# Kernel optimization log

Measured on AMD Instinct MI355X. Metric: run time of the kernel, lower is better.

## Reference

```python
import jax, jax.numpy as jnp
import numpy as np

# pywt Wavelet('db4') decomposition filters (8 taps)
DEC_LO = jnp.array([-0.010597401784997278, 0.032883011666982945, 0.030841381835986965,
                    -0.18703481171888114, -0.02798376941698385, 0.6308807679295904,
                    0.7148465705525415, 0.23037781330885523], dtype=jnp.float32)
DEC_HI = jnp.array([-0.23037781330885523, 0.7148465705525415, -0.6308807679295904,
                    -0.02798376941698385, 0.18703481171888114, 0.030841381835986965,
                    -0.032883011666982945, -0.010597401784997278], dtype=jnp.float32)
FLEN = 8
LEVEL = 3


def _dwt_last(x, f):
    """Single-level DWT along last axis, pywt 'symmetric' mode.
    out[i] = sum_k f[k] * ext[2i+1-k] (true convolution, downsample by 2)."""
    p = FLEN - 1
    pad = [(0, 0)] * (x.ndim - 1) + [(p, p)]
    xp = jnp.pad(x, pad, mode='symmetric')[..., 1:]
    n = x.shape[-1]
    out_len = (n + FLEN - 1) // 2
    f_rev = f[::-1]
    y = f_rev[0] * xp[..., 0:2 * out_len:2]
    for j in range(1, FLEN):  # fixed 8-tap loop
        y = y + f_rev[j] * xp[..., j:j + 2 * out_len:2]
    return y


def _dwt_h(x, f):
    # DWT along axis -2 (rows/H)
    return jnp.swapaxes(_dwt_last(jnp.swapaxes(x, -1, -2), f), -1, -2)


def _dwt2(x):
    # x: [B, H, W] -> (cA, cH, cV, cD), matching pywt dwt2 ('aa','da','ad','dd')
    lo_w = _dwt_last(x, DEC_LO)
    hi_w = _dwt_last(x, DEC_HI)
    cA = _dwt_h(lo_w, DEC_LO)  # low H,  low W
    cH = _dwt_h(lo_w, DEC_HI)  # high H, low W  (horizontal detail)
    cV = _dwt_h(hi_w, DEC_LO)  # low H,  high W (vertical detail)
    cD = _dwt_h(hi_w, DEC_HI)  # high H, high W (diagonal detail)
    return cA, cH, cV, cD


def setup_inputs() -> dict:
    key = jax.random.key(0)
    x = jax.random.normal(key, (16, 1, 1024, 1024), dtype=jnp.float32)
    return {"x": x}


def reference(x):
    # wavedec2 ordering: (cA_L, (cH_L, cV_L, cD_L), ..., (cH_1, cV_1, cD_1))
    a = x[:, 0]  # [B, H, W]
    details = []
    for _ in range(LEVEL):
        a, lh, hl, hh = _dwt2(a)
        details.insert(0, (lh, hl, hh))  # coarsest first, as pywt returns
    outs = [a[:, None]]  # [B,1,h,w]
    for lh, hl, hh in details:
        outs += [lh[:, None], hl[:, None], hh[:, None]]
    return tuple(outs)
```

## Files before the change

### kernel.cpp

```cpp
#include <hip/hip_runtime.h>

#define NT 512

__device__ __forceinline__ int refl(int i, int n) {
    i = (i < 0) ? (-i - 1) : i;
    i = (i >= n) ? (2 * n - 1 - i) : i;
    return i;
}

__device__ __forceinline__ unsigned bpack(float lo, float hi) {
    union { float f; unsigned u; } a, b;
    a.f = lo; b.f = hi;
    const unsigned ua = (a.u + 0x7FFFu + ((a.u >> 16) & 1u)) >> 16;
    const unsigned ub = (b.u + 0x7FFFu + ((b.u >> 16) & 1u)) & 0xFFFF0000u;
    return ua | ub;
}
__device__ __forceinline__ float b_lo(unsigned u) {
    union { unsigned u; float f; } x; x.u = u << 16; return x.f;
}
__device__ __forceinline__ float b_hi(unsigned u) {
    union { unsigned u; float f; } x; x.u = u & 0xFFFF0000u; return x.f;
}

__global__ __launch_bounds__(NT, 8)
void dwt2_fused(const float* __restrict__ in, int n, int ldin, int inb,
                int m, int nty, int ntx,
                float* __restrict__ oA, int ldA, int Ab,
                float* __restrict__ oH, float* __restrict__ oV,
                float* __restrict__ oD)
{
    constexpr float LOF[8] = {
        -0.010597401784997278f,  0.032883011666982945f,
         0.030841381835986965f, -0.18703481171888114f,
        -0.02798376941698385f,   0.6308807679295904f,
         0.7148465705525415f,    0.23037781330885523f };
    constexpr float HIF[8] = {
        -0.23037781330885523f,   0.7148465705525415f,
        -0.6308807679295904f,   -0.02798376941698385f,
         0.18703481171888114f,   0.030841381835986965f,
        -0.032883011666982945f, -0.010597401784997278f };

    __shared__ unsigned s[70 * 36];

    const int G = gridDim.x;
    const int q = G >> 3, rm = G & 7;
    const int xcd = blockIdx.x & 7, pos = blockIdx.x >> 3;
    const int i = xcd * q + (xcd < rm ? xcd : rm) + pos;
    const int ty = i % nty;
    const int t2 = i / nty;
    const int tx = t2 % ntx;
    const int b  = t2 / ntx;

    const int tid = threadIdx.x;
    const int c0 = tx * 32, r0 = ty * 32;
    const float* Ain = in + b * inb;

    const int rb  = 2 * r0 - 6;
    const int cw0 = 2 * c0 - 8;

    const bool interior = (rb >= 0) && (rb + 69 < n) && (cw0 >= 0) && (cw0 + 71 < n);

    const int tr0 = tid >> 3, g0 = tid & 7;
    const bool has2 = (tid < 48);
    const int tr1 = 64 + (tid >> 3), g1 = tid & 7;

    float v0[16], v1[16];
    if (interior) {
        const float* p0 = Ain + (rb + tr0) * ldin + (cw0 + 8 * g0);
        const float4 a0 = ((const float4*)p0)[0];
        const float4 a1 = ((const float4*)p0)[1];
        const float4 a2 = ((const float4*)p0)[2];
        const float4 a3 = ((const float4*)p0)[3];
        v0[0]=a0.x; v0[1]=a0.y; v0[2]=a0.z; v0[3]=a0.w;
        v0[4]=a1.x; v0[5]=a1.y; v0[6]=a1.z; v0[7]=a1.w;
        v0[8]=a2.x; v0[9]=a2.y; v0[10]=a2.z; v0[11]=a2.w;
        v0[12]=a3.x; v0[13]=a3.y; v0[14]=a3.z; v0[15]=a3.w;
        if (has2) {
            const float* p1 = Ain + (rb + tr1) * ldin + (cw0 + 8 * g1);
            const float4 b0 = ((const float4*)p1)[0];
            const float4 b1 = ((const float4*)p1)[1];
            const float4 b2 = ((const float4*)p1)[2];
            const float4 b3 = ((const float4*)p1)[3];
            v1[0]=b0.x; v1[1]=b0.y; v1[2]=b0.z; v1[3]=b0.w;
            v1[4]=b1.x; v1[5]=b1.y; v1[6]=b1.z; v1[7]=b1.w;
            v1[8]=b2.x; v1[9]=b2.y; v1[10]=b2.z; v1[11]=b2.w;
            v1[12]=b3.x; v1[13]=b3.y; v1[14]=b3.z; v1[15]=b3.w;
        }
    } else {
        const float* row0 = Ain + refl(rb + tr0, n) * ldin;
        const int cb0 = cw0 + 8 * g0;
        #pragma unroll
        for (int u = 0; u < 16; ++u) v0[u] = row0[refl(cb0 + u, n)];
        if (has2) {
            const float* row1 = Ain + refl(rb + tr1, n) * ldin;
            const int cb1 = cw0 + 8 * g1;
            #pragma unroll
            for (int u = 0; u < 16; ++u) v1[u] = row1[refl(cb1 + u, n)];
        }
    }

    {
        unsigned w[4];
        #pragma unroll
        for (int d = 0; d < 4; ++d) {
            float lo = 0.f, hi = 0.f;
            #pragma unroll
            for (int k = 0; k < 8; ++k) {
                const float x = v0[2 * d + 9 - k];
                lo += LOF[k] * x;
                hi += HIF[k] * x;
            }
            w[d] = bpack(lo, hi);
        }
        *(uint4*)&s[tr0 * 36 + 4 * g0] = make_uint4(w[0], w[1], w[2], w[3]);
    }
    if (has2) {
        unsigned w[4];
        #pragma unroll
        for (int d = 0; d < 4; ++d) {
            float lo = 0.f, hi = 0.f;
            #pragma unroll
            for (int k = 0; k < 8; ++k) {
                const float x = v1[2 * d + 9 - k];
                lo += LOF[k] * x;
                hi += HIF[k] * x;
            }
            w[d] = bpack(lo, hi);
        }
        *(uint4*)&s[tr1 * 36 + 4 * g1] = make_uint4(w[0], w[1], w[2], w[3]);
    }
    __syncthreads();

    const int c = tid & 31, pr = tid >> 5;
    float lov[10], hiv[10];
    #pragma unroll
    for (int j = 0; j < 10; ++j) {
        const unsigned u = s[(4 * pr + j) * 36 + c];
        lov[j] = b_lo(u); hiv[j] = b_hi(u);
    }
    float A0 = 0.f, H0 = 0.f, V0 = 0.f, D0 = 0.f;
    float A1 = 0.f, H1 = 0.f, V1 = 0.f, D1 = 0.f;
    #pragma unroll
    for (int k = 0; k < 8; ++k) {
        const float l0 = lov[7 - k], h0 = hiv[7 - k];
        const float l1 = lov[9 - k], h1 = hiv[9 - k];
        A0 += LOF[k] * l0;  H0 += HIF[k] * l0;
        V0 += LOF[k] * h0;  D0 += HIF[k] * h0;
        A1 += LOF[k] * l1;  H1 += HIF[k] * l1;
        V1 += LOF[k] * h1;  D1 += HIF[k] * h1;
    }
    const int gr = r0 + 2 * pr, gc = c0 + c;
    if (gc < m) {
        const int ob = b * (m * m);
        const int od = ob + gr * m + gc;
        if (gr < m) {
            oA[b * Ab + gr * ldA + gc] = A0;
            oH[od] = H0; oV[od] = V0; oD[od] = D0;
        }
        if (gr + 1 < m) {
            oA[b * Ab + (gr + 1) * ldA + gc] = A1;
            oH[od + m] = H1; oV[od + m] = V1; oD[od + m] = D1;
        }
    }
}

extern "C" void kernel_launch(void* const* d_in, const int* in_sizes, int n_in,
                              void* d_out, int out_size, void* d_ws, size_t ws_size,
                              hipStream_t stream) {
    const float* x = (const float*)d_in[0];
    float* out = (float*)d_out;
    float* ws  = (float*)d_ws;

    const int B = 16;
    const int n1 = 1024, m1 = 515;
    const int n2 = 515,  m2 = 261;
    const int n3 = 261,  m3 = 134;

    const int ld1 = 516, b1 = m1 * ld1;
    const int ld2 = 264, b2 = m2 * ld2;
    float* a1 = ws;
    float* a2 = ws + (size_t)b1 * B;

    const size_t sz1 = (size_t)B * m1 * m1;
    const size_t sz2 = (size_t)B * m2 * m2;
    const size_t sz3 = (size_t)B * m3 * m3;

    float* a3  = out;
    float* lh3 = a3  + sz3;
    float* hl3 = lh3 + sz3;
    float* hh3 = hl3 + sz3;
    float* lh2 = hh3 + sz3;
    float* hl2 = lh2 + sz2;
    float* hh2 = hl2 + sz2;
    float* lh1 = hh2 + sz2;
    float* hl1 = lh1 + sz1;
    float* hh1 = hl1 + sz1;

    const int t1 = (m1 + 31) / 32;
    const int t2_ = (m2 + 31) / 32;
    const int t3 = (m3 + 31) / 32;

    dim3 blk(NT);
    dim3 g1(t1 * t1 * B, 1, 1);
    dim3 g2(t2_ * t2_ * B, 1, 1);
    dim3 g3(t3 * t3 * B, 1, 1);

    dwt2_fused<<<g1, blk, 0, stream>>>(x,  n1, n1, n1 * n1,
                                       m1, t1, t1, a1, ld1, b1, lh1, hl1, hh1);
    dwt2_fused<<<g2, blk, 0, stream>>>(a1, n2, ld1, b1,
                                       m2, t2_, t2_, a2, ld2, b2, lh2, hl2, hh2);
    dwt2_fused<<<g3, blk, 0, stream>>>(a2, n3, ld2, b2,
                                       m3, t3, t3, out, m3, m3 * m3, lh3, hl3, hh3);
}
```

Before: 58.35 us.

## Enlarge DWT tiles to 64x64 outputs with 1024-thread blocks

Each block now produces a 64x64 output tile instead of 32x32 and runs 1024 threads. Each thread filters 16 input columns in the horizontal pass and two output columns in the vertical pass. The larger tile cuts the relative cost of re-reading the 8-tap halo and uses wider shared-memory reads. The filter taps move from in-kernel constexpr arrays to __constant__ memory. In exchange there are fewer blocks, especially at level 3, more padded work on edge tiles, higher register pressure, and the launch bound of 8 blocks of 1024 threads per CU cannot actually be met.

```diff
diff --git a/kernel.cpp b/kernel.cpp
--- a/kernel.cpp
+++ b/kernel.cpp
@@ -1,6 +1,6 @@
 #include <hip/hip_runtime.h>
 
-#define NT 512
+#define NT 1024
 
 __device__ __forceinline__ int refl(int i, int n) {
     i = (i < 0) ? (-i - 1) : i;
@@ -20,6 +20,98 @@
 }
 __device__ __forceinline__ float b_hi(unsigned u) {
     union { unsigned u; float f; } x; x.u = u & 0xFFFF0000u; return x.f;
+}
+
+__device__ __constant__ const float LOF[8] = {
+    -0.010597401784997278f,  0.032883011666982945f,
+     0.030841381835986965f, -0.18703481171888114f,
+    -0.02798376941698385f,   0.6308807679295904f,
+     0.7148465705525415f,    0.23037781330885523f };
+__device__ __constant__ const float HIF[8] = {
+    -0.23037781330885523f,   0.7148465705525415f,
+    -0.6308807679295904f,   -0.02798376941698385f,
+     0.18703481171888114f,   0.030841381835986965f,
+    -0.032883011666982945f, -0.010597401784997278f };
+
+template<bool FAST>
+__device__ __forceinline__ void itemA(int item, const float* __restrict__ Ain,
+                                      int n, int ldin, int rb, int cw0,
+                                      unsigned* __restrict__ s)
+{
+    const int tr = item >> 3, g = item & 7;
+    const int cw = cw0 + 16 * g;
+    float v[24];
+    if (FAST) {
+        const float* p = Ain + (rb + tr) * ldin + cw;
+        #pragma unroll
+        for (int j = 0; j < 6; ++j) {
+            const float4 t4 = *(const float4*)(p + 4 * j);
+            v[4*j] = t4.x; v[4*j+1] = t4.y; v[4*j+2] = t4.z; v[4*j+3] = t4.w;
+        }
+    } else {
+        const float* row = Ain + refl(rb + tr, n) * ldin;
+        #pragma unroll
+        for (int u = 0; u < 24; ++u) v[u] = row[refl(cw + u, n)];
+    }
+    unsigned w[8];
+    #pragma unroll
+    for (int d = 0; d < 8; ++d) {
+        float lo = 0.f, hi = 0.f;
+        #pragma unroll
+        for (int k = 0; k < 8; ++k) {
+            const float x = v[2 * d + 9 - k];
+            lo += LOF[k] * x;
+            hi += HIF[k] * x;
+        }
+        w[d] = bpack(lo, hi);
+    }
+    unsigned* dst = &s[tr * 68 + 8 * g];
+    *(uint4*)(dst)     = make_uint4(w[0], w[1], w[2], w[3]);
+    *(uint4*)(dst + 4) = make_uint4(w[4], w[5], w[6], w[7]);
+}
+
+__device__ __forceinline__ void itemB(int c2, int pr, const unsigned* __restrict__ s,
+                                      int r0, int c0, int m,
+                                      float* __restrict__ oA, int ldA, int oaB,
+                                      float* __restrict__ oH, float* __restrict__ oV,
+                                      float* __restrict__ oD, int obB)
+{
+    uint2 u[10];
+    #pragma unroll
+    for (int j = 0; j < 10; ++j)
+        u[j] = *(const uint2*)&s[(4 * pr + j) * 68 + 2 * c2];
+    const int gr = r0 + 2 * pr;
+    #pragma unroll
+    for (int col = 0; col < 2; ++col) {
+        const int gc = c0 + 2 * c2 + col;
+        if (gc >= m) continue;
+        float lov[10], hiv[10];
+        #pragma unroll
+        for (int j = 0; j < 10; ++j) {
+            const unsigned uu = col ? u[j].y : u[j].x;
+            lov[j] = b_lo(uu); hiv[j] = b_hi(uu);
+        }
+        float A0 = 0.f, H0 = 0.f, V0 = 0.f, D0 = 0.f;
+        float A1 = 0.f, H1 = 0.f, V1 = 0.f, D1 = 0.f;
+        #pragma unroll
+        for (int k = 0; k < 8; ++k) {
+            const float l0 = lov[7 - k], h0 = hiv[7 - k];
+            const float l1 = lov[9 - k], h1 = hiv[9 - k];
+            A0 += LOF[k] * l0;  H0 += HIF[k] * l0;
+            V0 += LOF[k] * h0;  D0 += HIF[k] * h0;
+            A1 += LOF[k] * l1;  H1 += HIF[k] * l1;
+            V1 += LOF[k] * h1;  D1 += HIF[k] * h1;
+        }
+        const int od = obB + gr * m + gc;
+        if (gr < m) {
+            oA[oaB + gr * ldA + gc] = A0;
+            oH[od] = H0; oV[od] = V0; oD[od] = D0;
+        }
+        if (gr + 1 < m) {
+            oA[oaB + (gr + 1) * ldA + gc] = A1;
+            oH[od + m] = H1; oV[od + m] = V1; oD[od + m] = D1;
+        }
+    }
 }
 
 __global__ __launch_bounds__(NT, 8)
@@ -29,18 +121,7 @@
                 float* __restrict__ oH, float* __restrict__ oV,
                 float* __restrict__ oD)
 {
-    constexpr float LOF[8] = {
-        -0.010597401784997278f,  0.032883011666982945f,
-         0.030841381835986965f, -0.18703481171888114f,
-        -0.02798376941698385f,   0.6308807679295904f,
-         0.7148465705525415f,    0.23037781330885523f };
-    constexpr float HIF[8] = {
-        -0.23037781330885523f,   0.7148465705525415f,
-        -0.6308807679295904f,   -0.02798376941698385f,
-         0.18703481171888114f,   0.030841381835986965f,
-        -0.032883011666982945f, -0.010597401784997278f };
-
-    __shared__ unsigned s[70 * 36];
+    __shared__ unsigned s[134 * 68];
 
     const int G = gridDim.x;
     const int q = G >> 3, rm = G & 7;
@@ -52,116 +133,26 @@
     const int b  = t2 / ntx;
 
     const int tid = threadIdx.x;
-    const int c0 = tx * 32, r0 = ty * 32;
+    const int c0 = tx * 64, r0 = ty * 64;
     const float* Ain = in + b * inb;
 
     const int rb  = 2 * r0 - 6;
     const int cw0 = 2 * c0 - 8;
 
-    const bool interior = (rb >= 0) && (rb + 69 < n) && (cw0 >= 0) && (cw0 + 71 < n);
-
-    const int tr0 = tid >> 3, g0 = tid & 7;
-    const bool has2 = (tid < 48);
-    const int tr1 = 64 + (tid >> 3), g1 = tid & 7;
-
-    float v0[16], v1[16];
+    const bool interior = (rb >= 0) && (rb + 133 < n) &&
+                          (cw0 >= 0) && (2 * c0 + 127 < n);
+
     if (interior) {
-        const float* p0 = Ain + (rb + tr0) * ldin + (cw0 + 8 * g0);
-        const float4 a0 = ((const float4*)p0)[0];
-        const float4 a1 = ((const float4*)p0)[1];
-        const float4 a2 = ((const float4*)p0)[2];
-        const float4 a3 = ((const float4*)p0)[3];
-        v0[0]=a0.x; v0[1]=a0.y; v0[2]=a0.z; v0[3]=a0.w;
-        v0[4]=a1.x; v0[5]=a1.y; v0[6]=a1.z; v0[7]=a1.w;
-        v0[8]=a2.x; v0[9]=a2.y; v0[10]=a2.z; v0[11]=a2.w;
-        v0[12]=a3.x; v0[13]=a3.y; v0[14]=a3.z; v0[15]=a3.w;
-        if (has2) {
-            const float* p1 = Ain + (rb + tr1) * ldin + (cw0 + 8 * g1);
-            const float4 b0 = ((const float4*)p1)[0];
-            const float4 b1 = ((const float4*)p1)[1];
-            const float4 b2 = ((const float4*)p1)[2];
-            const float4 b3 = ((const float4*)p1)[3];
-            v1[0]=b0.x; v1[1]=b0.y; v1[2]=b0.z; v1[3]=b0.w;
-            v1[4]=b1.x; v1[5]=b1.y; v1[6]=b1.z; v1[7]=b1.w;
-            v1[8]=b2.x; v1[9]=b2.y; v1[10]=b2.z; v1[11]=b2.w;
-            v1[12]=b3.x; v1[13]=b3.y; v1[14]=b3.z; v1[15]=b3.w;
-        }
+        itemA<true>(tid, Ain, n, ldin, rb, cw0, s);
+        if (tid < 48) itemA<true>(tid + 1024, Ain, n, ldin, rb, cw0, s);
     } else {
-        const float* row0 = Ain + refl(rb + tr0, n) * ldin;
-        const int cb0 = cw0 + 8 * g0;
-        #pragma unroll
-        for (int u = 0; u < 16; ++u) v0[u] = row0[refl(cb0 + u, n)];
-        if (has2) {
-            const float* row1 = Ain + refl(rb + tr1, n) * ldin;
-            const int cb1 = cw0 + 8 * g1;
-            #pragma unroll
-            for (int u = 0; u < 16; ++u) v1[u] = row1[refl(cb1 + u, n)];
-        }
-    }
-
-    {
-        unsigned w[4];
-        #pragma unroll
-        for (int d = 0; d < 4; ++d) {
-            float lo = 0.f, hi = 0.f;
-            #pragma unroll
-            for (int k = 0; k < 8; ++k) {
-                const float x = v0[2 * d + 9 - k];
-                lo += LOF[k] * x;
-                hi += HIF[k] * x;
-            }
-            w[d] = bpack(lo, hi);
-        }
-        *(uint4*)&s[tr0 * 36 + 4 * g0] = make_uint4(w[0], w[1], w[2], w[3]);
-    }
-    if (has2) {
-        unsigned w[4];
-        #pragma unroll
-        for (int d = 0; d < 4; ++d) {
-            float lo = 0.f, hi = 0.f;
-            #pragma unroll
-            for (int k = 0; k < 8; ++k) {
-                const float x = v1[2 * d + 9 - k];
-                lo += LOF[k] * x;
-                hi += HIF[k] * x;
-            }
-            w[d] = bpack(lo, hi);
-        }
-        *(uint4*)&s[tr1 * 36 + 4 * g1] = make_uint4(w[0], w[1], w[2], w[3]);
+        itemA<false>(tid, Ain, n, ldin, rb, cw0, s);
+        if (tid < 48) itemA<false>(tid + 1024, Ain, n, ldin, rb, cw0, s);
     }
     __syncthreads();
 
-    const int c = tid & 31, pr = tid >> 5;
-    float lov[10], hiv[10];
-    #pragma unroll
-    for (int j = 0; j < 10; ++j) {
-        const unsigned u = s[(4 * pr + j) * 36 + c];
-        lov[j] = b_lo(u); hiv[j] = b_hi(u);
-    }
-    float A0 = 0.f, H0 = 0.f, V0 = 0.f, D0 = 0.f;
-    float A1 = 0.f, H1 = 0.f, V1 = 0.f, D1 = 0.f;
-    #pragma unroll
-    for (int k = 0; k < 8; ++k) {
-        const float l0 = lov[7 - k], h0 = hiv[7 - k];
-        const float l1 = lov[9 - k], h1 = hiv[9 - k];
-        A0 += LOF[k] * l0;  H0 += HIF[k] * l0;
-        V0 += LOF[k] * h0;  D0 += HIF[k] * h0;
-        A1 += LOF[k] * l1;  H1 += HIF[k] * l1;
-        V1 += LOF[k] * h1;  D1 += HIF[k] * h1;
-    }
-    const int gr = r0 + 2 * pr, gc = c0 + c;
-    if (gc < m) {
-        const int ob = b * (m * m);
-        const int od = ob + gr * m + gc;
-        if (gr < m) {
-            oA[b * Ab + gr * ldA + gc] = A0;
-            oH[od] = H0; oV[od] = V0; oD[od] = D0;
-        }
-        if (gr + 1 < m) {
-            oA[b * Ab + (gr + 1) * ldA + gc] = A1;
-            oH[od + m] = H1; oV[od + m] = V1; oD[od + m] = D1;
-        }
-    }
+    const int c2 = tid & 31, pr = tid >> 5;
+    itemB(c2, pr, s, r0, c0, m, oA, ldA, b * Ab, oH, oV, oD, b * m * m);
 }
 
 extern "C" void kernel_launch(void* const* d_in, const int* in_sizes, int n_in,
@@ -196,9 +187,9 @@
     float* hl1 = lh1 + sz1;
     float* hh1 = hl1 + sz1;
 
-    const int t1 = (m1 + 31) / 32;
-    const int t2_ = (m2 + 31) / 32;
-    const int t3 = (m3 + 31) / 32;
+    const int t1 = (m1 + 63) / 64;
+    const int t2_ = (m2 + 63) / 64;
+    const int t3 = (m3 + 63) / 64;
 
     dim3 blk(NT);
     dim3 g1(t1 * t1 * B, 1, 1);
```

New measurement: 100.4 us. 72.0% more time.

## Split level-1 DWT into separate horizontal and vertical pass kernels via workspace

Applied to the files above, without the earlier changes.

The first-level 2D DWT is no longer a single fused tiled kernel. It now runs as two kernels: a horizontal pass that writes bf16-packed lo/hi rows to a workspace, and a vertical pass that reads columns and writes all four subbands. Each kernel splits threads into an interior fast path and a reflect-padded edge path, and batches are chunked to fit the workspace. Levels 2 and 3 keep the fused kernel, with the filter taps moved to constant memory. The split removes the halo recomputation and the shared-memory sync, but adds a full intermediate round trip through global memory and an extra launch.

```diff
diff --git a/kernel.cpp b/kernel.cpp
--- a/kernel.cpp
+++ b/kernel.cpp
@@ -1,6 +1,7 @@
 #include <hip/hip_runtime.h>
 
-#define NT 512
+#define NT 256
+#define NTF 512
 
 __device__ __forceinline__ int refl(int i, int n) {
     i = (i < 0) ? (-i - 1) : i;
@@ -22,24 +23,142 @@
     union { unsigned u; float f; } x; x.u = u & 0xFFFF0000u; return x.f;
 }
 
-__global__ __launch_bounds__(NT, 8)
+__device__ __constant__ const float LOF[8] = {
+    -0.010597401784997278f,  0.032883011666982945f,
+     0.030841381835986965f, -0.18703481171888114f,
+    -0.02798376941698385f,   0.6308807679295904f,
+     0.7148465705525415f,    0.23037781330885523f };
+__device__ __constant__ const float HIF[8] = {
+    -0.23037781330885523f,   0.7148465705525415f,
+    -0.6308807679295904f,   -0.02798376941698385f,
+     0.18703481171888114f,   0.030841381835986965f,
+    -0.032883011666982945f, -0.010597401784997278f };
+
+__device__ __forceinline__ void hconv8(const float v[24], unsigned w[8]) {
+    #pragma unroll
+    for (int d = 0; d < 8; ++d) {
+        float lo = 0.f, hi = 0.f;
+        #pragma unroll
+        for (int k = 0; k < 8; ++k) {
+            const float x = v[2 * d + 9 - k];
+            lo += LOF[k] * x;
+            hi += HIF[k] * x;
+        }
+        w[d] = bpack(lo, hi);
+    }
+}
+
+__global__ __launch_bounds__(NT)
+void dwt_h(const float* __restrict__ in, int n, int ldin, int inb,
+           unsigned* __restrict__ op, int ldo, int ob,
+           int rows, int ng, int Tint, int total)
+{
+    const int t = blockIdx.x * NT + threadIdx.x;
+    if (t >= total) return;
+
+    int g, row, b;
+    float v[24];
+    if (t < Tint) {
+        const int ngi = ng - 2;
+        g = 1 + t % ngi;
+        const int rr = t / ngi;
+        row = rr % rows;
+        b = rr / rows;
+        const float* base = in + b * inb + row * ldin + (16 * g - 8);
+        #pragma unroll
+        for (int j = 0; j < 6; ++j) {
+            const float4 t4 = *(const float4*)(base + 4 * j);
+            v[4*j] = t4.x; v[4*j+1] = t4.y; v[4*j+2] = t4.z; v[4*j+3] = t4.w;
+        }
+    } else {
+        const int e = t - Tint;
+        g = (e & 1) ? (ng - 1) : 0;
+        const int rr = e >> 1;
+        row = rr % rows;
+        b = rr / rows;
+        const float* base = in + b * inb + row * ldin;
+        const int cb = 16 * g - 8;
+        #pragma unroll
+        for (int u = 0; u < 24; ++u) v[u] = base[refl(cb + u, n)];
+    }
+
+    unsigned w[8];
+    hconv8(v, w);
+    unsigned* o = op + b * ob + row * ldo + 8 * g;
+    *(uint4*)(o) = make_uint4(w[0], w[1], w[2], w[3]);
+    if (8 * g + 7 < ldo)
+        *(uint4*)(o + 4) = make_uint4(w[4], w[5], w[6], w[7]);
+}
+
+__global__ __launch_bounds__(NT)
+void dwt_v(const unsigned* __restrict__ inp, int ldi, int ib, int n,
+           int m, int wcols,
+           float* __restrict__ oA, int ldA, int Ab,
+           float* __restrict__ oH, float* __restrict__ oVb,
+           float* __restrict__ oD, int db,
+           int nfast, int Tint, int total)
+{
+    const int t = blockIdx.x * NT + threadIdx.x;
+    if (t >= total) return;
+
+    int c, r2, b;
+    unsigned u[10];
+    if (t < Tint) {
+        c = t % wcols;
+        const int rr = t / wcols;
+        r2 = 2 + rr % nfast;
+        b = rr / nfast;
+        const unsigned* colp = inp + b * ib + c + (4 * r2 - 6) * ldi;
+        #pragma unroll
+        for (int j = 0; j < 10; ++j) u[j] = colp[j * ldi];
+    } else {
+        const int e = t - Tint;
+        c = e % wcols;
+        const int rr = e / wcols;
+        const int nsl = rr;
+        const int nrp = (m + 1) / 2;
+        const int nslow = nrp - nfast - 2 + 2;
+        const int which = nsl % nslow;
+        b = nsl / nslow;
+        r2 = (which < 2) ? which : (nfast + which);
+        const unsigned* colp = inp + b * ib + c;
+        const int rbase = 4 * r2 - 6;
+        #pragma unroll
+        for (int j = 0; j < 10; ++j) u[j] = colp[refl(rbase + j, n) * ldi];
+    }
+
+    float lov[10], hiv[10];
+    #pragma unroll
+    for (int j = 0; j < 10; ++j) { lov[j] = b_lo(u[j]); hiv[j] = b_hi(u[j]); }
+
+    float A0 = 0.f, H0 = 0.f, V0 = 0.f, D0 = 0.f;
+    float A1 = 0.f, H1 = 0.f, V1 = 0.f, D1 = 0.f;
+    #pragma unroll
+    for (int k = 0; k < 8; ++k) {
+        const float l0 = lov[7 - k], h0 = hiv[7 - k];
+        const float l1 = lov[9 - k], h1 = hiv[9 - k];
+        A0 += LOF[k] * l0;  H0 += HIF[k] * l0;
+        V0 += LOF[k] * h0;  D0 += HIF[k] * h0;
+        A1 += LOF[k] * l1;  H1 += HIF[k] * l1;
+        V1 += LOF[k] * h1;  D1 += HIF[k] * h1;
+    }
+    const int gr = 2 * r2;
+    const int od = b * db + gr * wcols + c;
+    oA[b * Ab + gr * ldA + c] = A0;
+    oH[od] = H0; oVb[od] = V0; oD[od] = D0;
+    if (gr + 1 < m) {
+        oA[b * Ab + (gr + 1) * ldA + c] = A1;
+        oH[od + wcols] = H1; oVb[od + wcols] = V1; oD[od + wcols] = D1;
+    }
+}
+
+__global__ __launch_bounds__(NTF, 8)
 void dwt2_fused(const float* __restrict__ in, int n, int ldin, int inb,
                 int m, int nty, int ntx,
                 float* __restrict__ oA, int ldA, int Ab,
                 float* __restrict__ oH, float* __restrict__ oV,
                 float* __restrict__ oD)
 {
-    constexpr float LOF[8] = {
-        -0.010597401784997278f,  0.032883011666982945f,
-         0.030841381835986965f, -0.18703481171888114f,
-        -0.02798376941698385f,   0.6308807679295904f,
-         0.7148465705525415f,    0.23037781330885523f };
-    constexpr float HIF[8] = {
-        -0.23037781330885523f,   0.7148465705525415f,
-        -0.6308807679295904f,   -0.02798376941698385f,
-         0.18703481171888114f,   0.030841381835986965f,
-        -0.032883011666982945f, -0.010597401784997278f };
-
     __shared__ unsigned s[70 * 36];
 
     const int G = gridDim.x;
@@ -57,7 +176,6 @@
 
     const int rb  = 2 * r0 - 6;
     const int cw0 = 2 * c0 - 8;
-
     const bool interior = (rb >= 0) && (rb + 69 < n) && (cw0 >= 0) && (cw0 + 71 < n);
 
     const int tr0 = tid >> 3, g0 = tid & 7;
@@ -169,18 +287,14 @@
                               hipStream_t stream) {
     const float* x = (const float*)d_in[0];
     float* out = (float*)d_out;
-    float* ws  = (float*)d_ws;
 
     const int B = 16;
     const int n1 = 1024, m1 = 515;
     const int n2 = 515,  m2 = 261;
     const int n3 = 261,  m3 = 134;
 
-    const int ld1 = 516, b1 = m1 * ld1;
-    const int ld2 = 264, b2 = m2 * ld2;
-    float* a1 = ws;
-    float* a2 = ws + (size_t)b1 * B;
-
+    const int ld1 = 516;
+    const int ld2 = 264;
     const size_t sz1 = (size_t)B * m1 * m1;
     const size_t sz2 = (size_t)B * m2 * m2;
     const size_t sz3 = (size_t)B * m3 * m3;
@@ -194,21 +308,58 @@
     float* hh2 = hl2 + sz2;
     float* lh1 = hh2 + sz2;
     float* hl1 = lh1 + sz1;
-    float* hh1 = hl1 + sz1;
-
-    const int t1 = (m1 + 31) / 32;
+    float* hh1 = lh1 + 2 * sz1;
+
+    const size_t perb = ((size_t)ld1 * n1 + (size_t)ld1 * m1) * 4;
+    int nb = B;
+    while (nb > 1 && (size_t)nb * perb > ws_size) nb >>= 1;
+
+    unsigned* X = (unsigned*)d_ws;
+    float*    Y = (float*)((unsigned*)d_ws + (size_t)ld1 * n1 * nb);
+
+    const int ng1 = 65;
+    const int h1_Tint  = n1 * (ng1 - 2) * nb;
+    const int h1_total = h1_Tint + n1 * 2 * nb;
+    const int nrp1 = (m1 + 1) / 2;
+    const int nfast1 = (n1 - 4) / 4 - 1;
+    const int nslow1 = nrp1 - nfast1 - 2 + 2;
+    const int v1_Tint  = m1 * nfast1 * nb;
+    const int v1_total = v1_Tint + m1 * nslow1 * nb;
+
     const int t2_ = (m2 + 31) / 32;
-    const int t3 = (m3 + 31) / 32;
-
-    dim3 blk(NT);
-    dim3 g1(t1 * t1 * B, 1, 1);
-    dim3 g2(t2_ * t2_ * B, 1, 1);
-    dim3 g3(t3 * t3 * B, 1, 1);
-
-    dwt2_fused<<<g1, blk, 0, stream>>>(x,  n1, n1, n1 * n1,
-                                       m1, t1, t1, a1, ld1, b1, lh1, hl1, hh1);
-    dwt2_fused<<<g2, blk, 0, stream>>>(a1, n2, ld1, b1,
-                                       m2, t2_, t2_, a2, ld2, b2, lh2, hl2, hh2);
-    dwt2_fused<<<g3, blk, 0, stream>>>(a2, n3, ld2, b2,
-                                       m3, t3, t3, out, m3, m3 * m3, lh3, hl3, hh3);
-}
+    const int t3  = (m3 + 31) / 32;
+
+    const int a1b = ld1 * m1;
+    const int a2b = ld2 * m2;
+
+    for (int g0 = 0; g0 < B; g0 += nb) {
+        const float* xin = x + (size_t)g0 * n1 * n1;
+
+        dwt_h<<<dim3((h1_total + NT - 1) / NT), dim3(NT), 0, stream>>>(
+            xin, n1, n1, n1 * n1,
+            X, ld1, ld1 * n1,
+            n1, ng1, h1_Tint, h1_total);
+
+        dwt_v<<<dim3((v1_total + NT - 1) / NT), dim3(NT), 0, stream>>>(
+            X, ld1, ld1 * n1, n1,
+            m1, m1,
+            Y, ld1, a1b,
+            lh1 + (size_t)g0 * m1 * m1, hl1 + (size_t)g0 * m1 * m1,
+            hh1 + (size_t)g0 * m1 * m1, m1 * m1,
+            nfast1, v1_Tint, v1_total);
+
+        dwt2_fused<<<dim3(t2_ * t2_ * nb), dim3(NTF), 0, stream>>>(
+            Y, n2, ld1, a1b,
+            m2, t2_, t2_,
+            (float*)X, ld2, a2b,
+            lh2 + (size_t)g0 * m2 * m2, hl2 + (size_t)g0 * m2 * m2,
+            hh2 + (size_t)g0 * m2 * m2);
+
+        dwt2_fused<<<dim3(t3 * t3 * nb), dim3(NTF), 0, stream>>>(
+            (float*)X, n3, ld2, a2b,
+            m3, t3, t3,
+            a3 + (size_t)g0 * m3 * m3, m3, m3 * m3,
+            lh3 + (size_t)g0 * m3 * m3, hl3 + (size_t)g0 * m3 * m3,
+            hh3 + (size_t)g0 * m3 * m3);
+    }
+}
```

After: 70.38 us. 20.6% more time.
